# Kernel optimization log

Hardware: AMD Instinct MI355X
Metric: run time of the kernel (lower is better)

## Reference

```python
import jax, jax.numpy as jnp
import numpy as np

LOG_0 = -1.0e30          # finite stand-in for log(0); avoids -inf NaNs under vjp
ACTIVE = -1.0e29         # anything above this is an 'active' beam
PRUNE_LOGIT = -9.0       # original skips extensions with log-prob <= -9


def _decode_one(probs, length, beam_width, blank_index):
    """CTC prefix beam search for one example. probs: [T, V] log-probs."""
    T, V = probs.shape
    Bw = beam_width
    t_idx = jnp.arange(T)
    v_idx = jnp.arange(V)
    b_idx = jnp.arange(Bw)

    def step(carry, inp):
        t, pr = inp  # pr: [V] log-probs at time t
        prefixes, lens, p_b, p_nb = carry
        p_tot = jnp.logaddexp(p_b, p_nb)
        act = p_tot > ACTIVE
        last = jnp.where(lens > 0, prefixes[b_idx, jnp.maximum(lens - 1, 0)], blank_index)
        # match[i, j]: prefix_i == prefix_j + [last_i]  (tree parent relation)
        eq = (prefixes[:, None, :] == prefixes[None, :, :]) | (t_idx[None, None, :] >= lens[None, :, None])
        match = eq.all(-1) & (lens[:, None] == lens[None, :] + 1) & act[None, :] & act[:, None]
        has_par = match.any(axis=1)
        par = jnp.argmax(match, axis=1)
        par_prev = jnp.where(has_par, jnp.where(last == last[par], p_b[par], p_tot[par]), LOG_0)
        # kept-beam (branch) update: label prob merges parent contribution, then emits last label
        cont_nb = jnp.where(lens > 0, jnp.logaddexp(p_nb, par_prev) + pr[last], LOG_0)
        cont_b = p_tot + pr[blank_index]
        # extension candidates [Bw, V]: p = probs[l] + (p_blank if l == last else p_total)
        prev_ext = jnp.where(v_idx[None, :] == last[:, None], p_b[:, None], p_tot[:, None])
        ext_nb = pr[None, :] + prev_ext
        # child already a live beam -> merged via branch update above, skip extension
        child_in = (jnp.zeros((Bw, V), jnp.int32).at[par, last].add(has_par.astype(jnp.int32)) > 0)
        bad = (v_idx[None, :] == blank_index) | (pr[None, :] <= PRUNE_LOGIT) | child_in | ~act[:, None]
        ext_nb = jnp.where(bad, LOG_0, ext_nb)
        # prune all candidates (Bw continuations + Bw*V extensions) to top beam_width
        all_pb = jnp.concatenate([cont_b, jnp.full((Bw * V,), LOG_0, cont_b.dtype)])
        all_pnb = jnp.concatenate([cont_nb, ext_nb.reshape(-1)])
        _, top = jax.lax.top_k(jnp.logaddexp(all_pb, all_pnb), Bw)
        is_ext = top >= Bw
        src = jnp.where(is_ext, (top - Bw) // V, top)
        lab = ((top - Bw) % V).astype(jnp.int32)  # garbage for continuations, masked below
        new_pref = prefixes[src]
        src_len = lens[src]
        put = is_ext[:, None] & (t_idx[None, :] == src_len[:, None])
        new_pref = jnp.where(put, lab[:, None], new_pref)
        new_lens = src_len + is_ext.astype(jnp.int32)
        new_pb = all_pb[top]
        new_pnb = all_pnb[top]
        live = t < length
        return (jnp.where(live, new_pref, prefixes),
                jnp.where(live, new_lens, lens),
                jnp.where(live, new_pb, p_b),
                jnp.where(live, new_pnb, p_nb)), None

    init = (jnp.full((Bw, T), -1, jnp.int32),
            jnp.zeros((Bw,), jnp.int32),
            jnp.full((Bw,), LOG_0, probs.dtype).at[0].set(0.0),  # root: blank prob = log(1)
            jnp.full((Bw,), LOG_0, probs.dtype))
    (prefixes, lens, p_b, p_nb), _ = jax.lax.scan(step, init, (t_idx, probs))
    totals = jnp.logaddexp(p_b, p_nb)
    best = jnp.argmax(totals)
    seq = jnp.where(t_idx < lens[best], prefixes[best], 0)
    return seq, lens[best], totals[best]


def setup_inputs() -> dict:
    key = jax.random.key(0)
    k1, k2 = jax.random.split(key)
    B, T, V = 128, 256, 128
    logits = jax.random.normal(k1, (B, T, V), jnp.float32) * 2.0
    probabilities = jax.nn.log_softmax(logits, axis=-1)  # module consumes log-probs
    lengths = jax.random.randint(k2, (B,), 1, T + 1, dtype=jnp.int32)
    return {"probabilities": probabilities, "lengths": lengths,
            "beam_width": 8, "blank_index": 0}


def reference(probabilities, lengths, beam_width, blank_index):
    dec = jax.vmap(lambda p, L: _decode_one(p, L, beam_width, blank_index))(probabilities, lengths)
    seqs, dec_lens, _scores = dec
    # decoded label sequences padded with 0 (to T), plus per-example decoded lengths
    return seqs, dec_lens
```

## Files before the change

kernel.cpp:

```cpp
#include <hip/hip_runtime.h>
#include <math.h>

#define LOG0f (-1.0e30f)
#define ACTIVE_TH (-1.0e29f)
#define PRUNE_TH (-9.0f)
#define VCAB 128
#define HSZ 4096
#define HMASK (HSZ - 1)
#define MAXN 2052
#define HEMPTY 0xFFFFFFFFu

__device__ __forceinline__ float lae(float a, float b) {
    float mx = fmaxf(a, b);
    float d = fabsf(a - b);
    return mx + log1pf(expf(-d));
}
__device__ __forceinline__ unsigned mono(float f) {
    unsigned u = __float_as_uint(f);
    return (u & 0x80000000u) ? ~u : (u | 0x80000000u);
}
__device__ __forceinline__ float mono_inv(unsigned m) {
    unsigned u = (m & 0x80000000u) ? (m & 0x7FFFFFFFu) : ~m;
    return __uint_as_float(u);
}
__device__ __forceinline__ unsigned rlaneu(unsigned x, int l) {
    return (unsigned)__builtin_amdgcn_readlane((int)x, l);
}
__device__ __forceinline__ float rlanef(float x, int l) {
    return __uint_as_float(rlaneu(__float_as_uint(x), l));
}
__device__ __forceinline__ unsigned sel8u(const unsigned a[8], unsigned s) {
    unsigned r = a[0];
#pragma unroll
    for (int j = 1; j < 8; ++j) r = (s == (unsigned)j) ? a[j] : r;
    return r;
}

__device__ __forceinline__ unsigned wred_max_u32(unsigned x) {
    unsigned y;
    y = (unsigned)__builtin_amdgcn_update_dpp(0, (int)x, 0x111, 0xf, 0xf, false);
    x = (y > x) ? y : x;
    y = (unsigned)__builtin_amdgcn_update_dpp(0, (int)x, 0x112, 0xf, 0xf, false);
    x = (y > x) ? y : x;
    y = (unsigned)__builtin_amdgcn_update_dpp(0, (int)x, 0x114, 0xf, 0xf, false);
    x = (y > x) ? y : x;
    y = (unsigned)__builtin_amdgcn_update_dpp(0, (int)x, 0x118, 0xf, 0xf, false);
    x = (y > x) ? y : x;
    y = (unsigned)__builtin_amdgcn_update_dpp(0, (int)x, 0x142, 0xa, 0xf, false);
    x = (y > x) ? y : x;
    y = (unsigned)__builtin_amdgcn_update_dpp(0, (int)x, 0x143, 0xc, 0xf, false);
    x = (y > x) ? y : x;
    return (unsigned)__builtin_amdgcn_readlane((int)x, 63);
}

#define REP8(X) X(0) X(1) X(2) X(3) X(4) X(5) X(6) X(7)
#define REP7(X) X(1) X(2) X(3) X(4) X(5) X(6) X(7)
#define SEL8N(out, s, n)                                                        \
    do {                                                                        \
        out = n##_0;                                                            \
        out = ((s) == 1u) ? n##_1 : out; out = ((s) == 2u) ? n##_2 : out;       \
        out = ((s) == 3u) ? n##_3 : out; out = ((s) == 4u) ? n##_4 : out;       \
        out = ((s) == 5u) ? n##_5 : out; out = ((s) == 6u) ? n##_6 : out;       \
        out = ((s) == 7u) ? n##_7 : out;                                        \
    } while (0)

__global__ __launch_bounds__(64)
void ctc_beam_kernel(const float* __restrict__ probs, const int* __restrict__ lengths,
                     const int* __restrict__ blank_p, int* __restrict__ out_seq,
                     int* __restrict__ out_len, int T) {
    __shared__ unsigned hsh[HSZ];
    __shared__ unsigned nodeinfo[MAXN];
    __shared__ int sh_seq[256];

    const int lane = threadIdx.x;
    const int b = blockIdx.x;
    const int blank = blank_p[0];
    const int length = lengths[b];
    const float* __restrict__ P = probs + (size_t)b * T * VCAB;
    const float4* __restrict__ P4 = (const float4*)P;
    const int own = lane & 7;
    const int slice = lane >> 3;
    const int vbase = slice * 16;

    for (int i = lane; i < HSZ; i += 64) hsh[i] = HEMPTY;
    __syncthreads();

    unsigned node8[8], par8[8], len8[8], last8[8];
#pragma unroll
    for (int j = 0; j < 8; ++j) {
        node8[j] = 0; par8[j] = 0xFFFu; len8[j] = 0; last8[j] = (unsigned)blank;
    }
    float pb_own = (own == 0) ? 0.0f : LOG0f;
    float pnb_own = LOG0f;
    int len_own = 0, last_own = blank;
    unsigned node_own = 0, par_own = 0xFFFu;

    float4 s0, s1, s2, s3;
    float prL, prH;
    {
        int base4 = (vbase >> 2);
        s0 = P4[base4]; s1 = P4[base4 + 1]; s2 = P4[base4 + 2]; s3 = P4[base4 + 3];
        prL = P[lane]; prH = P[64 + lane];
    }

#pragma clang loop unroll(disable)
    for (int t = 0; t < length; ++t) {
        const int tn = (t + 1 < length) ? (t + 1) : (length - 1);
        float4 n0, n1, n2, n3;
        float nprL, nprH;
        {
            int base4 = tn * 32 + (vbase >> 2);
            n0 = P4[base4]; n1 = P4[base4 + 1]; n2 = P4[base4 + 2]; n3 = P4[base4 + 3];
            nprL = P[(size_t)tn * VCAB + lane];
            nprH = P[(size_t)tn * VCAB + 64 + lane];
        }

        float pt_own = lae(pb_own, pnb_own);
        unsigned long long bal = __ballot(pt_own > ACTIVE_TH);
        unsigned actmask = (unsigned)bal & 0xFFu;
        bool act_own = (actmask >> own) & 1u;

#define TBL(j) float pb8_##j = rlanef(pb_own, j); float pt8_##j = rlanef(pt_own, j);
        REP8(TBL)
#undef TBL
        float prB = (blank < 64) ? rlanef(prL, blank) : rlanef(prH, blank - 64);
#define PRV(j)                                                                  \
        float prv8_##j;                                                         \
        {                                                                       \
            int lj = (int)last8[j];                                             \
            float a_ = rlanef(prL, lj & 63), c_ = rlanef(prH, lj & 63);         \
            prv8_##j = (lj < 64) ? a_ : c_;                                     \
        }
        REP8(PRV)
#undef PRV

        int p_own = 0;
        bool matched = false;
        {
            bool gate = act_own && (len_own > 0);
#define PM(j)                                                                   \
            {                                                                   \
                bool m_ = gate && ((actmask >> j) & 1u) && (node8[j] == par_own); \
                if (m_) { p_own = j; matched = true; }                          \
            }
            REP8(PM)
#undef PM
        }
        float pbp = pb8_0, ptp = pt8_0;
        int lastp = (int)last8[0];
#define PSEL(j)                                                                 \
        {                                                                       \
            bool m_ = (p_own == j);                                             \
            pbp = m_ ? pb8_##j : pbp;                                           \
            ptp = m_ ? pt8_##j : ptp;                                           \
            lastp = m_ ? (int)last8[j] : lastp;                                 \
        }
        REP7(PSEL)
#undef PSEL
        float pprev = matched ? ((last_own == lastp) ? pbp : ptp) : LOG0f;
        float prLast = prv8_0;
#define PLSEL(j) prLast = (own == j) ? prv8_##j : prLast;
        REP7(PLSEL)
#undef PLSEL

        float contb_own = pt_own + prB;
        float contnb_own = (len_own > 0) ? (lae(pnb_own, pprev) + prLast) : LOG0f;
        float tot_own = lae(contb_own, contnb_own);

        unsigned claimed16 = 0;
#pragma unroll
        for (int j = 0; j < 8; ++j) {
            bool mj = ((actmask >> j) & 1u) && act_own && (node_own == par8[j]);
            bool ins = ((last8[j] >> 4) == (unsigned)slice);
            claimed16 |= (mj && ins) ? (1u << (last8[j] & 15u)) : 0u;
        }

        unsigned long long K[17];
#define MAKEK(c, pv)                                                                     \
        {                                                                                \
            int v = vbase + (c);                                                         \
            float prev = (v == last_own) ? pb_own : pt_own;                              \
            float val = (pv) + prev;                                                     \
            bool bad = (v == blank) | ((pv) <= PRUNE_TH) | (!act_own) |                  \
                       (bool)((claimed16 >> (c)) & 1u);                                  \
            if (bad) val = LOG0f;                                                        \
            K[c] = (((unsigned long long)mono(val)) << 32) |                             \
                   (unsigned)~(8u + (unsigned)(own * VCAB + v));                         \
        }
        MAKEK(0, s0.x) MAKEK(1, s0.y) MAKEK(2, s0.z) MAKEK(3, s0.w)
        MAKEK(4, s1.x) MAKEK(5, s1.y) MAKEK(6, s1.z) MAKEK(7, s1.w)
        MAKEK(8, s2.x) MAKEK(9, s2.y) MAKEK(10, s2.z) MAKEK(11, s2.w)
        MAKEK(12, s3.x) MAKEK(13, s3.y) MAKEK(14, s3.z) MAKEK(15, s3.w)
#undef MAKEK
        K[16] = (lane < 8)
                    ? ((((unsigned long long)mono(tot_own)) << 32) | (unsigned)~(unsigned)lane)
                    : 0ull;

        unsigned long long a1 = 0ull, a2 = 0ull, a3 = 0ull;
        unsigned long long b1 = 0ull, b2 = 0ull, b3 = 0ull;
#define INSC(t1v, t2v, t3v, key)                                                \
        {                                                                       \
            unsigned long long k_ = (key);                                      \
            bool g1 = k_ > t1v, g2 = k_ > t2v, g3 = k_ > t3v;                   \
            unsigned long long x1 = g1 ? k_ : t1v;                              \
            unsigned long long x2 = g1 ? t1v : (g2 ? k_ : t2v);                 \
            t3v = (g1 | g2) ? t2v : (g3 ? k_ : t3v);                            \
            t1v = x1; t2v = x2;                                                 \
        }
        INSC(a1, a2, a3, K[0])  INSC(a1, a2, a3, K[2])  INSC(a1, a2, a3, K[4])
        INSC(a1, a2, a3, K[6])  INSC(a1, a2, a3, K[8])  INSC(a1, a2, a3, K[10])
        INSC(a1, a2, a3, K[12]) INSC(a1, a2, a3, K[14]) INSC(a1, a2, a3, K[16])
        INSC(b1, b2, b3, K[1])  INSC(b1, b2, b3, K[3])  INSC(b1, b2, b3, K[5])
        INSC(b1, b2, b3, K[7])  INSC(b1, b2, b3, K[9])  INSC(b1, b2, b3, K[11])
        INSC(b1, b2, b3, K[13]) INSC(b1, b2, b3, K[15])
#undef INSC
        unsigned long long m1, m2, m3;
        {
            unsigned long long u = (a1 < b1) ? a1 : b1;
            m1 = (a1 < b1) ? b1 : a1;
            unsigned long long v = (a2 < b2) ? b2 : a2;
            unsigned long long w = (a2 < b2) ? a2 : b2;
            m2 = (u < v) ? v : u;
            unsigned long long mn = (u < v) ? u : v;
            unsigned long long X = (a2 > b1) ? a3 : ((b2 > a1) ? b3 : 0ull);
            unsigned long long wX = (w < X) ? X : w;
            m3 = (mn < wX) ? wX : mn;
        }

        unsigned long long W = ~0ull;
        unsigned selh_0, selh_1, selh_2, selh_3, selh_4, selh_5, selh_6, selh_7;
        unsigned sell_0, sell_1, sell_2, sell_3, sell_4, sell_5, sell_6, sell_7;
        bool dead = false;
#define ROUND(r)                                                                         \
        do {                                                                             \
            unsigned long long c = (m1 < W) ? m1 : ((m2 < W) ? m2 : ((m3 < W) ? m3 : 0ull)); \
            bool need = (c == 0ull) && !dead;                                            \
            if (__any(need)) {                                                           \
                if (need) {                                                              \
                    c = 0ull;                                                            \
                    _Pragma("unroll")                                                    \
                    for (int k = 0; k < 17; ++k) {                                       \
                        bool g = (K[k] < W) && (K[k] > c);                               \
                        c = g ? K[k] : c;                                                \
                    }                                                                    \
                    if (c == 0ull) dead = true;                                          \
                    else { m1 = c; m2 = ~0ull; m3 = ~0ull; }                             \
                }                                                                        \
            }                                                                            \
            unsigned ch = (unsigned)(c >> 32), cl = (unsigned)c;                         \
            unsigned M = wred_max_u32(ch);                                               \
            unsigned long long tb = __ballot(ch == M);                                   \
            unsigned L;                                                                  \
            if (__builtin_popcountll(tb) == 1) {                                         \
                L = rlaneu(cl, __builtin_ctzll(tb));                                     \
            } else {                                                                     \
                unsigned lo2 = (ch == M) ? cl : 0u;                                      \
                L = wred_max_u32(lo2);                                                   \
            }                                                                            \
            W = (((unsigned long long)M) << 32) | L;                                     \
            selh_##r = M; sell_##r = L;                                                  \
        } while (0);
        ROUND(0) ROUND(1) ROUND(2) ROUND(3) ROUND(4) ROUND(5) ROUND(6) ROUND(7)
#undef ROUND

#define CBT(j) float cb8_##j = rlanef(contb_own, j); float cn8_##j = rlanef(contnb_own, j);
        REP8(CBT)
#undef CBT

        unsigned myM, myL;
        SEL8N(myM, (unsigned)own, selh);
        SEL8N(myL, (unsigned)own, sell);
        unsigned sel = ~myL;
        bool iscont = sel < 8u;
        unsigned e = sel - 8u;
        unsigned s = iscont ? sel : (e >> 7);
        unsigned lab = e & 127u;
        unsigned nd = sel8u(node8, s);
        unsigned pr = sel8u(par8, s);
        unsigned ln = sel8u(len8, s);
        unsigned la = sel8u(last8, s);
        float cbs, cns;
        SEL8N(cbs, s, cb8);
        SEL8N(cns, s, cn8);
        float npb_own = iscont ? cbs : LOG0f;
        float npnb_own = iscont ? cns : mono_inv(myM);
        unsigned A = iscont ? ((nd << 12) | pr) : nd;
        unsigned Bv = iscont ? ((ln << 7) | la) : (((ln + 1u) << 7) | lab);
        unsigned long long extbal = __ballot(!iscont);
        unsigned extmask = (unsigned)extbal & 0xFFu;

        unsigned insRes = 0;
        if ((extmask >> lane) & 1u) {
            unsigned preid = 1u + 8u * (unsigned)t + (unsigned)lane;
            unsigned hkey = (nd << 7) | lab;
            unsigned entry = (hkey << 12) | preid;
            unsigned h = ((hkey * 2654435761u) >> 20) & HMASK;
            for (;;) {
                unsigned prev = atomicCAS(&hsh[h], HEMPTY, entry);
                if (prev == HEMPTY) { nodeinfo[preid] = hkey; insRes = preid; break; }
                if ((prev >> 12) == hkey) { insRes = prev & 0xFFFu; break; }
                h = (h + 1) & HMASK;
            }
        }
#pragma unroll
        for (int r = 0; r < 8; ++r) {
            unsigned Ar = rlaneu(A, r);
            unsigned Br = rlaneu(Bv, r);
            unsigned nd2 = Ar >> 12;
            if ((extmask >> r) & 1u) nd2 = rlaneu(insRes, r);
            node8[r] = nd2; par8[r] = Ar & 0xFFFu;
            len8[r] = Br >> 7; last8[r] = Br & 127u;
        }
        node_own = sel8u(node8, (unsigned)own);
        par_own = sel8u(par8, (unsigned)own);
        len_own = (int)sel8u(len8, (unsigned)own);
        last_own = (int)sel8u(last8, (unsigned)own);
        pb_own = npb_own; pnb_own = npnb_own;

        s0 = n0; s1 = n1; s2 = n2; s3 = n3;
        prL = nprL; prH = nprH;
    }

    unsigned fh, fl;
    {
        float tot = lae(pb_own, pnb_own);
        fh = (lane < 8) ? mono(tot) : 0u;
        fl = (lane < 8) ? ~(unsigned)lane : 0u;
    }
    {
        unsigned M = wred_max_u32(fh);
        unsigned lo2 = (fh == M) ? fl : 0u;
        fl = wred_max_u32(lo2);
    }
    const int best = (int)(~fl);
    int L = 0;
    unsigned c = 0;
#pragma unroll
    for (int j = 0; j < 8; ++j)
        if (best == j) { L = (int)len8[j]; c = node8[j]; }
    if (lane == 0) {
        for (int k = L - 1; k >= 0; --k) {
            unsigned info = nodeinfo[c];
            sh_seq[k] = (int)(info & 127u);
            c = info >> 7;
        }
    }
    __syncthreads();
    for (int j = lane; j < T; j += 64)
        out_seq[(size_t)b * T + j] = (j < L) ? sh_seq[j] : 0;
    if (lane == 0) out_len[b] = L;
}

extern "C" void kernel_launch(void* const* d_in, const int* in_sizes, int n_in,
                              void* d_out, int out_size, void* d_ws, size_t ws_size,
                              hipStream_t stream) {
    const float* probs = (const float*)d_in[0];
    const int* lengths = (const int*)d_in[1];
    const int* blank_p = (const int*)d_in[3];
    const int B = in_sizes[1];
    const int T = in_sizes[0] / (B * VCAB);
    int* out = (int*)d_out;
    ctc_beam_kernel<<<B, 64, 0, stream>>>(probs, lengths, blank_p, out,
                                          out + (size_t)B * T, T);
}
```

Before: 1.175 ms.

## Use 32-bit keys with position tags in top-k selection and prefetch two steps ahead

The per-lane top-3 candidate tracking now stores 32-bit score keys plus a small position index instead of 64-bit packed keys. Each selection round pops the winner from the local list and recomputes the next candidate from the stored keys only when the list runs empty, which should cut 64-bit compare/select work and register pressure. The probability row prefetch is also deepened from one timestep to two, to hide global load latency in the serial time loop. The cost is more live registers for the second prefetch buffer and somewhat more complex tie-breaking logic.

```diff
diff --git a/kernel.cpp b/kernel.cpp
--- a/kernel.cpp
+++ b/kernel.cpp
@@ -81,6 +81,7 @@
     const int own = lane & 7;
     const int slice = lane >> 3;
     const int vbase = slice * 16;
+    const unsigned KLB = ~(8u + (unsigned)(own * VCAB + vbase));
 
     for (int i = lane; i < HSZ; i += 64) hsh[i] = HEMPTY;
     __syncthreads();
@@ -95,24 +96,29 @@
     int len_own = 0, last_own = blank;
     unsigned node_own = 0, par_own = 0xFFFu;
 
-    float4 s0, s1, s2, s3;
-    float prL, prH;
+    float4 s0, s1, s2, s3, m0, m1_, m2_, m3_;
+    float prL, prH, mprL, mprH;
     {
         int base4 = (vbase >> 2);
         s0 = P4[base4]; s1 = P4[base4 + 1]; s2 = P4[base4 + 2]; s3 = P4[base4 + 3];
         prL = P[lane]; prH = P[64 + lane];
+        int t1 = (1 < length) ? 1 : (length - 1);
+        int b1 = t1 * 32 + (vbase >> 2);
+        m0 = P4[b1]; m1_ = P4[b1 + 1]; m2_ = P4[b1 + 2]; m3_ = P4[b1 + 3];
+        mprL = P[(size_t)t1 * VCAB + lane];
+        mprH = P[(size_t)t1 * VCAB + 64 + lane];
     }
 
 #pragma clang loop unroll(disable)
     for (int t = 0; t < length; ++t) {
-        const int tn = (t + 1 < length) ? (t + 1) : (length - 1);
-        float4 n0, n1, n2, n3;
-        float nprL, nprH;
+        const int t2 = (t + 2 < length) ? (t + 2) : (length - 1);
+        float4 q0, q1, q2, q3;
+        float qprL, qprH;
         {
-            int base4 = tn * 32 + (vbase >> 2);
-            n0 = P4[base4]; n1 = P4[base4 + 1]; n2 = P4[base4 + 2]; n3 = P4[base4 + 3];
-            nprL = P[(size_t)tn * VCAB + lane];
-            nprH = P[(size_t)tn * VCAB + 64 + lane];
+            int base4 = t2 * 32 + (vbase >> 2);
+            q0 = P4[base4]; q1 = P4[base4 + 1]; q2 = P4[base4 + 2]; q3 = P4[base4 + 3];
+            qprL = P[(size_t)t2 * VCAB + lane];
+            qprH = P[(size_t)t2 * VCAB + 64 + lane];
         }
 
         float pt_own = lae(pb_own, pnb_own);
@@ -175,7 +181,8 @@
             claimed16 |= (mj && ins) ? (1u << (last8[j] & 15u)) : 0u;
         }
 
-        unsigned long long K[17];
+        unsigned kh_0, kh_1, kh_2, kh_3, kh_4, kh_5, kh_6, kh_7, kh_8, kh_9,
+                 kh_10, kh_11, kh_12, kh_13, kh_14, kh_15, kh_16;
 #define MAKEK(c, pv)                                                                     \
         {                                                                                \
             int v = vbase + (c);                                                         \
@@ -184,84 +191,118 @@
             bool bad = (v == blank) | ((pv) <= PRUNE_TH) | (!act_own) |                  \
                        (bool)((claimed16 >> (c)) & 1u);                                  \
             if (bad) val = LOG0f;                                                        \
-            K[c] = (((unsigned long long)mono(val)) << 32) |                             \
-                   (unsigned)~(8u + (unsigned)(own * VCAB + v));                         \
+            kh_##c = mono(val);                                                          \
         }
         MAKEK(0, s0.x) MAKEK(1, s0.y) MAKEK(2, s0.z) MAKEK(3, s0.w)
         MAKEK(4, s1.x) MAKEK(5, s1.y) MAKEK(6, s1.z) MAKEK(7, s1.w)
         MAKEK(8, s2.x) MAKEK(9, s2.y) MAKEK(10, s2.z) MAKEK(11, s2.w)
         MAKEK(12, s3.x) MAKEK(13, s3.y) MAKEK(14, s3.z) MAKEK(15, s3.w)
 #undef MAKEK
-        K[16] = (lane < 8)
-                    ? ((((unsigned long long)mono(tot_own)) << 32) | (unsigned)~(unsigned)lane)
-                    : 0ull;
-
-        unsigned long long a1 = 0ull, a2 = 0ull, a3 = 0ull;
-        unsigned long long b1 = 0ull, b2 = 0ull, b3 = 0ull;
-#define INSC(t1v, t2v, t3v, key)                                                \
+        kh_16 = (lane < 8) ? mono(tot_own) : 0u;
+
+        unsigned a1v = 0u, a1p = 31u, a2v = 0u, a2p = 31u, a3v = 0u, a3p = 31u;
+        unsigned b1v = 0u, b1p = 31u, b2v = 0u, b2p = 31u, b3v = 0u, b3p = 31u;
+#define CINS(c1v, c1p, c2v, c2p, c3v, c3p, V, PR)                               \
         {                                                                       \
-            unsigned long long k_ = (key);                                      \
-            bool g1 = k_ > t1v, g2 = k_ > t2v, g3 = k_ > t3v;                   \
-            unsigned long long x1 = g1 ? k_ : t1v;                              \
-            unsigned long long x2 = g1 ? t1v : (g2 ? k_ : t2v);                 \
-            t3v = (g1 | g2) ? t2v : (g3 ? k_ : t3v);                            \
-            t1v = x1; t2v = x2;                                                 \
-        }
-        INSC(a1, a2, a3, K[0])  INSC(a1, a2, a3, K[2])  INSC(a1, a2, a3, K[4])
-        INSC(a1, a2, a3, K[6])  INSC(a1, a2, a3, K[8])  INSC(a1, a2, a3, K[10])
-        INSC(a1, a2, a3, K[12]) INSC(a1, a2, a3, K[14]) INSC(a1, a2, a3, K[16])
-        INSC(b1, b2, b3, K[1])  INSC(b1, b2, b3, K[3])  INSC(b1, b2, b3, K[5])
-        INSC(b1, b2, b3, K[7])  INSC(b1, b2, b3, K[9])  INSC(b1, b2, b3, K[11])
-        INSC(b1, b2, b3, K[13]) INSC(b1, b2, b3, K[15])
-#undef INSC
-        unsigned long long m1, m2, m3;
+            unsigned v_ = (V); bool g1 = v_ > c1v, g2 = v_ > c2v, g3 = v_ > c3v; \
+            unsigned x1v = g1 ? v_ : c1v;  unsigned x1p = g1 ? (PR) : c1p;      \
+            unsigned x2v = g1 ? c1v : (g2 ? v_ : c2v);                          \
+            unsigned x2p = g1 ? c1p : (g2 ? (PR) : c2p);                        \
+            c3v = (g1 | g2) ? c2v : (g3 ? v_ : c3v);                            \
+            c3p = (g1 | g2) ? c2p : (g3 ? (PR) : c3p);                          \
+            c1v = x1v; c1p = x1p; c2v = x2v; c2p = x2p;                         \
+        }
+        CINS(a1v, a1p, a2v, a2p, a3v, a3p, kh_16, 0u)
+        CINS(a1v, a1p, a2v, a2p, a3v, a3p, kh_0, 1u)
+        CINS(a1v, a1p, a2v, a2p, a3v, a3p, kh_2, 3u)
+        CINS(a1v, a1p, a2v, a2p, a3v, a3p, kh_4, 5u)
+        CINS(a1v, a1p, a2v, a2p, a3v, a3p, kh_6, 7u)
+        CINS(a1v, a1p, a2v, a2p, a3v, a3p, kh_8, 9u)
+        CINS(a1v, a1p, a2v, a2p, a3v, a3p, kh_10, 11u)
+        CINS(a1v, a1p, a2v, a2p, a3v, a3p, kh_12, 13u)
+        CINS(a1v, a1p, a2v, a2p, a3v, a3p, kh_14, 15u)
+        CINS(b1v, b1p, b2v, b2p, b3v, b3p, kh_1, 2u)
+        CINS(b1v, b1p, b2v, b2p, b3v, b3p, kh_3, 4u)
+        CINS(b1v, b1p, b2v, b2p, b3v, b3p, kh_5, 6u)
+        CINS(b1v, b1p, b2v, b2p, b3v, b3p, kh_7, 8u)
+        CINS(b1v, b1p, b2v, b2p, b3v, b3p, kh_9, 10u)
+        CINS(b1v, b1p, b2v, b2p, b3v, b3p, kh_11, 12u)
+        CINS(b1v, b1p, b2v, b2p, b3v, b3p, kh_13, 14u)
+        CINS(b1v, b1p, b2v, b2p, b3v, b3p, kh_15, 16u)
+#undef CINS
+#define GTE(xv, xp, yv, yp) (((xv) > (yv)) || ((xv) == (yv) && (xp) < (yp)))
+        unsigned m1v, m1p, m2v, m2p, m3v, m3p;
         {
-            unsigned long long u = (a1 < b1) ? a1 : b1;
-            m1 = (a1 < b1) ? b1 : a1;
-            unsigned long long v = (a2 < b2) ? b2 : a2;
-            unsigned long long w = (a2 < b2) ? a2 : b2;
-            m2 = (u < v) ? v : u;
-            unsigned long long mn = (u < v) ? u : v;
-            unsigned long long X = (a2 > b1) ? a3 : ((b2 > a1) ? b3 : 0ull);
-            unsigned long long wX = (w < X) ? X : w;
-            m3 = (mn < wX) ? wX : mn;
-        }
-
-        unsigned long long W = ~0ull;
+            bool gA = GTE(a1v, a1p, b1v, b1p);
+            m1v = gA ? a1v : b1v; m1p = gA ? a1p : b1p;
+            unsigned uv = gA ? b1v : a1v, up = gA ? b1p : a1p;
+            bool gS = GTE(a2v, a2p, b2v, b2p);
+            unsigned vv = gS ? a2v : b2v, vp = gS ? a2p : b2p;
+            unsigned wv = gS ? b2v : a2v, wp = gS ? b2p : a2p;
+            bool gM = GTE(uv, up, vv, vp);
+            m2v = gM ? uv : vv; m2p = gM ? up : vp;
+            unsigned mnv = gM ? vv : uv, mnp = gM ? vp : up;
+            bool gX = GTE(a2v, a2p, b1v, b1p);
+            bool gY = GTE(b2v, b2p, a1v, a1p);
+            unsigned Xv = gX ? a3v : (gY ? b3v : 0u);
+            unsigned Xp = gX ? a3p : (gY ? b3p : 31u);
+            bool gW = GTE(wv, wp, Xv, Xp);
+            unsigned Yv = gW ? wv : Xv, Yp = gW ? wp : Xp;
+            bool gF = GTE(mnv, mnp, Yv, Yp);
+            m3v = gF ? mnv : Yv; m3p = gF ? mnp : Yp;
+        }
+#undef GTE
+
         unsigned selh_0, selh_1, selh_2, selh_3, selh_4, selh_5, selh_6, selh_7;
         unsigned sell_0, sell_1, sell_2, sell_3, sell_4, sell_5, sell_6, sell_7;
-        bool dead = false;
-#define ROUND(r)                                                                         \
-        do {                                                                             \
-            unsigned long long c = (m1 < W) ? m1 : ((m2 < W) ? m2 : ((m3 < W) ? m3 : 0ull)); \
-            bool need = (c == 0ull) && !dead;                                            \
-            if (__any(need)) {                                                           \
-                if (need) {                                                              \
-                    c = 0ull;                                                            \
-                    _Pragma("unroll")                                                    \
-                    for (int k = 0; k < 17; ++k) {                                       \
-                        bool g = (K[k] < W) && (K[k] > c);                               \
-                        c = g ? K[k] : c;                                                \
-                    }                                                                    \
-                    if (c == 0ull) dead = true;                                          \
-                    else { m1 = c; m2 = ~0ull; m3 = ~0ull; }                             \
-                }                                                                        \
-            }                                                                            \
-            unsigned ch = (unsigned)(c >> 32), cl = (unsigned)c;                         \
-            unsigned M = wred_max_u32(ch);                                               \
-            unsigned long long tb = __ballot(ch == M);                                   \
-            unsigned L;                                                                  \
-            if (__builtin_popcountll(tb) == 1) {                                         \
-                L = rlaneu(cl, __builtin_ctzll(tb));                                     \
-            } else {                                                                     \
-                unsigned lo2 = (ch == M) ? cl : 0u;                                      \
-                L = wred_max_u32(lo2);                                                   \
-            }                                                                            \
-            W = (((unsigned long long)M) << 32) | L;                                     \
-            selh_##r = M; sell_##r = L;                                                  \
+#define RS1(k)                                                                  \
+        {                                                                       \
+            unsigned kv = kh_##k; unsigned kcl = KLB - (unsigned)(k);           \
+            bool below = (kv < M) | ((kv == M) & (kcl < L));                    \
+            bool bet = below & ((kv > bv) | ((kv == bv) & (kcl > bcl)));        \
+            bv = bet ? kv : bv; bp = bet ? (unsigned)((k) + 1) : bp;            \
+            bcl = bet ? kcl : bcl;                                              \
+        }
+#define ROUND(r)                                                                \
+        do {                                                                    \
+            unsigned ch = m1v;                                                  \
+            unsigned cl = (m1p == 0u) ? ~(unsigned)own : (KLB - (m1p - 1u));    \
+            unsigned M = wred_max_u32(ch);                                      \
+            unsigned long long tb = __ballot(ch == M);                          \
+            unsigned L;                                                         \
+            if (__builtin_popcountll(tb) == 1) {                                \
+                L = rlaneu(cl, __builtin_ctzll(tb));                            \
+            } else {                                                            \
+                unsigned lo2 = (ch == M) ? cl : 0u;                             \
+                L = wred_max_u32(lo2);                                          \
+            }                                                                   \
+            selh_##r = M; sell_##r = L;                                         \
+            bool won = (ch == M) & (cl == L);                                   \
+            m1v = won ? m2v : m1v; m1p = won ? m2p : m1p;                       \
+            m2v = won ? m3v : m2v; m2p = won ? m3p : m2p;                       \
+            m3v = won ? 0u : m3v;  m3p = won ? 31u : m3p;                       \
+            bool under = won & (m1v == 0u);                                     \
+            if (__any(under)) {                                                 \
+                if (under) {         \
+                    unsigned bv = 0u, bp = 31u, bcl = 0u;                       \
+                    RS1(0) RS1(1) RS1(2) RS1(3) RS1(4) RS1(5) RS1(6) RS1(7)     \
+                    RS1(8) RS1(9) RS1(10) RS1(11) RS1(12) RS1(13) RS1(14)       \
+                    RS1(15)                                                     \
+                    {                                                           \
+                        unsigned kv = kh_16; unsigned kcl = ~(unsigned)own;     \
+                        bool below = (kv < M) | ((kv == M) & (kcl < L));        \
+                        bool bet = below &                                      \
+                                   ((kv > bv) | ((kv == bv) & (kcl > bcl)));    \
+                        bv = bet ? kv : bv; bp = bet ? 0u : bp;                 \
+                        bcl = bet ? kcl : bcl;                                  \
+                    }                                                           \
+                    m1v = bv; m1p = bp;            \
+                }                                                               \
+            }                                                                   \
         } while (0);
         ROUND(0) ROUND(1) ROUND(2) ROUND(3) ROUND(4) ROUND(5) ROUND(6) ROUND(7)
 #undef ROUND
+#undef RS1
 
 #define CBT(j) float cb8_##j = rlanef(contb_own, j); float cn8_##j = rlanef(contnb_own, j);
         REP8(CBT)
@@ -317,8 +358,10 @@
         last_own = (int)sel8u(last8, (unsigned)own);
         pb_own = npb_own; pnb_own = npnb_own;
 
-        s0 = n0; s1 = n1; s2 = n2; s3 = n3;
-        prL = nprL; prH = nprH;
+        s0 = m0; s1 = m1_; s2 = m2_; s3 = m3_;
+        prL = mprL; prH = mprH;
+        m0 = q0; m1_ = q1; m2_ = q2; m3_ = q3;
+        mprL = qprL; mprH = qprH;
     }
 
     unsigned fh, fl;
```

Result: no change. 1.181 ms (+0.5%).
